# Kernel optimization log

Hardware: AMD Instinct MI355X
Metric: run time of the kernel (lower is better)

Reference implementation:

```python
import jax, jax.numpy as jnp
import numpy as np

N_RAYS = 8192
M = 524288
GX, GY, GZ = 160, 160, 128
NFEAT = 12
POS_PE, VIEW_PE = 10, 4
WIDTH = 128
POS_DIM = 3 + 3 * POS_PE * 2      # 63
VIEW_DIM = 3 + 3 * VIEW_PE * 2    # 27
DIM0 = NFEAT + POS_DIM            # 75
ACT_SHIFT = float(np.log(1.0 / (1.0 - 1e-6) - 1.0))  # density bias shift from alpha_init
INTERVAL = 0.5                    # stepsize * voxel_size_ratio
XYZ_MIN, XYZ_MAX = -1.0, 1.0


def posemb(x, n_pe):
    # x: [N,3] -> [N, 3 + 3*n_pe*2], matching cat([x, sin(x*freq), cos(x*freq)])
    freq = 2.0 ** jnp.arange(n_pe, dtype=x.dtype)
    xf = (x[..., None] * freq).reshape(x.shape[0], -1)
    return jnp.concatenate([x, jnp.sin(xf), jnp.cos(xf)], axis=-1)


def trilinear(grid, xyz):
    # grid: [X,Y,Z,C]; xyz: [M,3] in world coords. align_corners=True bilinear (grid_sample).
    sz_f = jnp.array(grid.shape[:3], jnp.float32)
    sz_i = jnp.array(grid.shape[:3], jnp.int32)
    t = (xyz - XYZ_MIN) / (XYZ_MAX - XYZ_MIN) * (sz_f - 1.0)
    t = jnp.clip(t, 0.0, sz_f - 1.0)
    i0 = jnp.clip(jnp.floor(t).astype(jnp.int32), 0, sz_i - 2)
    f = t - i0.astype(t.dtype)
    out = jnp.zeros((xyz.shape[0], grid.shape[-1]), t.dtype)
    for dx in (0, 1):
        for dy in (0, 1):
            for dz in (0, 1):
                w = ((f[:, 0] if dx else 1.0 - f[:, 0])
                     * (f[:, 1] if dy else 1.0 - f[:, 1])
                     * (f[:, 2] if dz else 1.0 - f[:, 2]))
                out = out + w[:, None] * grid[i0[:, 0] + dx, i0[:, 1] + dy, i0[:, 2] + dz]
    return out


def mask_lookup(mask, xyz):
    # nearest-neighbor maskcache_lookup: ijk = round(xyz*scale + shift)
    sz_f = jnp.array(mask.shape, jnp.float32)
    scale = (sz_f - 1.0) / (XYZ_MAX - XYZ_MIN)
    shift = -XYZ_MIN * scale
    ijk = jnp.clip(jnp.round(xyz * scale + shift).astype(jnp.int32), 0,
                   jnp.array(mask.shape, jnp.int32) - 1)
    return mask[ijk[:, 0], ijk[:, 1], ijk[:, 2]]


def alphas2weights(alpha, ray_id, n_rays):
    # segmented T_i = prod_{j<i in ray}(1-alpha_j); weights = T*alpha (ray_id sorted)
    log1a = jnp.log(jnp.clip(1.0 - alpha, 1e-10, 1.0))
    excl = jnp.cumsum(log1a) - log1a                      # global exclusive cumsum
    seg_tot = jax.ops.segment_sum(log1a, ray_id, num_segments=n_rays)
    seg_start = jnp.cumsum(seg_tot) - seg_tot             # exclusive prefix over rays
    T = jnp.exp(excl - seg_start[ray_id])
    weights = T * alpha
    alphainv_last = jnp.exp(seg_tot)
    return weights, alphainv_last


def setup_inputs() -> dict:
    key = jax.random.key(0)
    ks = jax.random.split(key, 16)
    xyz = jax.random.uniform(ks[0], (M, 3), jnp.float32) * (XYZ_MAX - XYZ_MIN) + XYZ_MIN
    ray_id = jnp.sort(jax.random.randint(ks[1], (M,), 0, N_RAYS))
    viewdirs = jax.random.normal(ks[2], (N_RAYS, 3), jnp.float32)
    viewdirs = viewdirs / jnp.linalg.norm(viewdirs, axis=-1, keepdims=True)
    mask = jax.random.uniform(ks[3], (GX, GY, GZ)) > 0.1
    density = jax.random.normal(ks[4], (GX, GY, GZ), jnp.float32) * 0.5
    k0 = jax.random.normal(ks[5], (GX, GY, GZ, NFEAT), jnp.float32) * 0.1
    s = 0.05
    W0 = jax.random.normal(ks[6], (DIM0, WIDTH), jnp.float32) * s
    b0 = jnp.zeros((WIDTH,), jnp.float32)
    W1 = jax.random.normal(ks[7], (WIDTH, WIDTH), jnp.float32) * s
    b1 = jnp.zeros((WIDTH,), jnp.float32)
    W2 = jax.random.normal(ks[8], (WIDTH, WIDTH), jnp.float32) * s
    b2 = jnp.zeros((WIDTH,), jnp.float32)
    Wr = jax.random.normal(ks[9], (WIDTH + VIEW_DIM, 3), jnp.float32) * s
    br = jnp.zeros((3,), jnp.float32)
    return {"xyz": xyz, "ray_id": ray_id, "viewdirs": viewdirs, "mask": mask,
            "density": density, "k0": k0, "W0": W0, "b0": b0, "W1": W1, "b1": b1,
            "W2": W2, "b2": b2, "Wr": Wr, "br": br}


def reference(xyz, ray_id, viewdirs, mask, density, k0, W0, b0, W1, b1, W2, b2, Wr, br):
    # 1) empty-space skipping via mask cache (kept as multiplicative mask for static shapes)
    m = mask_lookup(mask, xyz).astype(xyz.dtype)
    # 2) trilinear density query + raw2alpha
    d = trilinear(density[..., None], xyz)[:, 0]
    alpha = 1.0 - (1.0 + jnp.exp(d + ACT_SHIFT)) ** (-INTERVAL)
    alpha = alpha * m
    # 3) segmented alpha compositing (Alphas2Weights)
    weights, alphainv_last = alphas2weights(alpha, ray_id, N_RAYS)
    # 4) feature query + view MLP -> rgb
    feat = trilinear(k0, xyz)                              # [M, NFEAT]
    h = jnp.concatenate([feat, posemb(xyz, POS_PE)], -1)   # [M, DIM0]
    h = jax.nn.relu(h @ W0 + b0)
    h = jax.nn.relu(h @ W1 + b1)
    h = jax.nn.relu(h @ W2 + b2)
    ve = posemb(viewdirs, VIEW_PE)[ray_id]                 # [M, VIEW_DIM]
    rgb = jax.nn.sigmoid(jnp.concatenate([h, ve], -1) @ Wr + br)
    # 5) composite per ray + white background
    rgb_marched = jax.ops.segment_sum(weights[:, None] * rgb, ray_id, num_segments=N_RAYS)
    rgb_marched = rgb_marched + alphainv_last[:, None] * 1.0
    return rgb_marched
```

## Files before the change

### kernel.cpp

```cpp
#include <hip/hip_runtime.h>
#include <hip/hip_bf16.h>

#define M_SAMPLES 524288
#define NRAYS 8192
#define GXD 160
#define GYD 160
#define GZD 128
#define GYZ (GYD*GZD)
#define NVOX (GXD*GYD*GZD)
#define ACT_SHIFT -13.81550955796f
#define ROWA 136
#define ROWB 136
#define SAMP 64

typedef __bf16 bf16x8 __attribute__((ext_vector_type(8)));
typedef float f32x4 __attribute__((ext_vector_type(4)));
typedef float f32x16 __attribute__((ext_vector_type(16)));
typedef float f32v2 __attribute__((ext_vector_type(2)));

static __device__ inline unsigned short f2bf(float f){
  __hip_bfloat16 h = __float2bfloat16(f);
  unsigned short u; __builtin_memcpy(&u, &h, 2); return u;
}
static __device__ inline float flo(unsigned int u){ return __uint_as_float(u << 16); }
static __device__ inline float fhi(unsigned int u){ return __uint_as_float(u & 0xffff0000u); }

#if defined(__has_builtin)
#if __has_builtin(__builtin_amdgcn_cvt_pk_bf16_f32)
#define HAVE_PK_BF16 1
#endif
#if __has_builtin(__builtin_amdgcn_cvt_pk_f32_fp8) && __has_builtin(__builtin_amdgcn_cvt_pk_fp8_f32)
#define HAVE_FP8 1
#endif
#endif

static __device__ inline unsigned int packbf(float a, float b){
#ifdef HAVE_PK_BF16
  typedef __bf16 bf16v2 __attribute__((ext_vector_type(2)));
  bf16v2 r = __builtin_amdgcn_cvt_pk_bf16_f32(a, b);
  unsigned int u; __builtin_memcpy(&u, &r, 4); return u;
#else
  return (unsigned int)f2bf(a) | ((unsigned int)f2bf(b) << 16);
#endif
}

struct Tri {
  int ix, iy, iz;
  float wx0, wx1, wy0, wy1, wz0, wz1;
};
static __device__ inline Tri tri_setup(float x, float y, float z){
  Tri t;
  float tx = (x+1.f)*0.5f*(float)(GXD-1); tx = fminf(fmaxf(tx,0.f),(float)(GXD-1));
  float ty = (y+1.f)*0.5f*(float)(GYD-1); ty = fminf(fmaxf(ty,0.f),(float)(GYD-1));
  float tz = (z+1.f)*0.5f*(float)(GZD-1); tz = fminf(fmaxf(tz,0.f),(float)(GZD-1));
  t.ix = min((int)tx, GXD-2); t.iy = min((int)ty, GYD-2); t.iz = min((int)tz, GZD-2);
  float fx = tx-t.ix, fy = ty-t.iy, fz = tz-t.iz;
  t.wx0 = 1.f-fx; t.wx1 = fx; t.wy0 = 1.f-fy; t.wy1 = fy; t.wz0 = 1.f-fz; t.wz1 = fz;
  return t;
}

#define NB_REPACK (NVOX/256)
#define NB_W      184
#define NB_RT     (NRAYS/256)
__global__ __launch_bounds__(256) void k_prep(
    const float* __restrict__ density, const float* __restrict__ k0,
    uint4* __restrict__ packed,
    const unsigned int* __restrict__ mw, int* __restrict__ flag,
    const float* __restrict__ W0, const float* __restrict__ W1,
    const float* __restrict__ W2, const float* __restrict__ Wr,
    const float* __restrict__ br,
    unsigned short* __restrict__ wt0, unsigned short* __restrict__ wt1,
    unsigned short* __restrict__ wt2, unsigned short* __restrict__ wtr,
    const float* __restrict__ vd, float* __restrict__ rayterm3)
{
  int b = blockIdx.x;
  if(b < NB_REPACK){
    int v = b*256 + threadIdx.x;
    const float4* kp = (const float4*)(k0 + (size_t)v*12);
    float4 a = kp[0], bb = kp[1], c = kp[2];
#ifdef HAVE_FP8
    uint4 o;
    o.x = __float_as_uint(density[v]);
    int w;
    w = __builtin_amdgcn_cvt_pk_fp8_f32(a.x, a.y, 0, false);
    w = __builtin_amdgcn_cvt_pk_fp8_f32(a.z, a.w, w, true);
    o.y = (unsigned int)w;
    w = __builtin_amdgcn_cvt_pk_fp8_f32(bb.x, bb.y, 0, false);
    w = __builtin_amdgcn_cvt_pk_fp8_f32(bb.z, bb.w, w, true);
    o.z = (unsigned int)w;
    w = __builtin_amdgcn_cvt_pk_fp8_f32(c.x, c.y, 0, false);
    w = __builtin_amdgcn_cvt_pk_fp8_f32(c.z, c.w, w, true);
    o.w = (unsigned int)w;
    packed[v] = o;
#else
    uint4 o0, o1;
    o0.x = __float_as_uint(density[v]);
    o0.y = packbf(a.x, a.y); o0.z = packbf(a.z, a.w); o0.w = packbf(bb.x, bb.y);
    o1.x = packbf(bb.z, bb.w); o1.y = packbf(c.x, c.y); o1.z = packbf(c.z, c.w);
    o1.w = 0;
    packed[(size_t)v*2]   = o0;
    packed[(size_t)v*2+1] = o1;
#endif
    return;
  }
  if(b == NB_REPACK){
    unsigned int v = mw[threadIdx.x & 63];
    unsigned long long any = __ballot(v > 1u);
    if(threadIdx.x == 0) *flag = (any != 0ull) ? 1 : 0;
    return;
  }
  if(b < NB_REPACK + 1 + NB_W){
    int t = (b - NB_REPACK - 1)*256 + threadIdx.x;
    if(t < 128*96){
      int n = t/96, k = t%96;
      wt0[t] = f2bf((k < 75) ? W0[k*128 + n] : 0.f);
    } else if(t < 128*96 + 16384){
      int j = t - 128*96; int n = j/128, k = j%128;
      wt1[j] = f2bf(W1[k*128 + n]);
    } else if(t < 128*96 + 32768){
      int j = t - 128*96 - 16384; int n = j/128, k = j%128;
      wt2[j] = f2bf(W2[k*128 + n]);
    } else if(t < 128*96 + 32768 + 16*128){
      int j = t - 128*96 - 32768; int n = j/128, k = j%128;
      wtr[j] = f2bf((n < 3) ? Wr[k*3 + n] : 0.f);
    }
    return;
  }
  int ray = (b - NB_REPACK - 1 - NB_W)*256 + threadIdx.x;
  if(ray >= NRAYS) return;
  float v0 = vd[ray*3+0], v1 = vd[ray*3+1], v2 = vd[ray*3+2];
  float vej[27];
  vej[0] = v0; vej[1] = v1; vej[2] = v2;
  #pragma unroll
  for(int ci = 0; ci < 3; ++ci){
    float xv = (ci == 0) ? v0 : ((ci == 1) ? v1 : v2);
    #pragma unroll
    for(int p = 0; p < 4; ++p){
      float arg = xv * (float)(1 << p);
      vej[3 + ci*4 + p]  = __sinf(arg);
      vej[15 + ci*4 + p] = __cosf(arg);
    }
  }
  float rt0 = br[0], rt1 = br[1], rt2 = br[2];
  #pragma unroll
  for(int j = 0; j < 27; ++j){
    const float* wr = Wr + (128 + j)*3;
    rt0 += vej[j]*wr[0]; rt1 += vej[j]*wr[1]; rt2 += vej[j]*wr[2];
  }
  rayterm3[ray*3+0] = rt0; rayterm3[ray*3+1] = rt1; rayterm3[ray*3+2] = rt2;
}

template<int KDIM, int SROW>
static __device__ __forceinline__ void mfma_layer(const unsigned short* src,
    const bf16x8* wf, f32x16& acc0, f32x16& acc1, int ln, int kh)
{
  constexpr int NS = KDIM/16;
  const unsigned short* abase0 = src + (ln)*SROW + kh*8;
  const unsigned short* abase1 = src + (32 + ln)*SROW + kh*8;
  f32x16 z = {0.f,0.f,0.f,0.f,0.f,0.f,0.f,0.f,0.f,0.f,0.f,0.f,0.f,0.f,0.f,0.f};
  acc0 = z; acc1 = z;
  __builtin_amdgcn_s_setprio(1);
  #pragma unroll
  for(int st = 0; st < NS; ++st){
    bf16x8 a0 = *(const bf16x8*)(abase0 + st*16);
    bf16x8 a1 = *(const bf16x8*)(abase1 + st*16);
    acc0 = __builtin_amdgcn_mfma_f32_32x32x16_bf16(wf[st], a0, acc0, 0, 0, 0);
    acc1 = __builtin_amdgcn_mfma_f32_32x32x16_bf16(wf[st], a1, acc1, 0, 0, 0);
  }
  __builtin_amdgcn_s_setprio(0);
}

template<int NS>
static __device__ __forceinline__ void load_wf(const unsigned short* wbase, bf16x8* wf){
  #pragma unroll
  for(int st = 0; st < NS; ++st) wf[st] = *(const bf16x8*)(wbase + st*16);
}

template<int DROW>
static __device__ __forceinline__ void epilogue(const f32x16& acc0, const f32x16& acc1,
    unsigned short* dst, const float* __restrict__ bias, int tile_n, int ln, int kh)
{
  float4 bv[4];
  #pragma unroll
  for(int g = 0; g < 4; ++g) bv[g] = *(const float4*)(bias + tile_n*32 + g*8 + kh*4);
  #pragma unroll
  for(int rep = 0; rep < 2; ++rep){
    const f32x16& acc = rep ? acc1 : acc0;
    int scol = rep*32 + ln;
    #pragma unroll
    for(int g = 0; g < 4; ++g){
      int n0 = tile_n*32 + g*8 + kh*4;
      unsigned int lo = packbf(fmaxf(acc[4*g+0] + bv[g].x, 0.f), fmaxf(acc[4*g+1] + bv[g].y, 0.f));
      unsigned int hi = packbf(fmaxf(acc[4*g+2] + bv[g].z, 0.f), fmaxf(acc[4*g+3] + bv[g].w, 0.f));
      unsigned long long o = (unsigned long long)lo | ((unsigned long long)hi << 32);
      *(unsigned long long*)(dst + scol*DROW + n0) = o;
    }
  }
}

template<int PACKED>
__global__ __launch_bounds__(256, 4) void k_mlp(const float* __restrict__ xyz,
    const uint4* __restrict__ packed,
    const float* __restrict__ density, const float* __restrict__ k0,
    const void* __restrict__ mask, const int* __restrict__ flag,
    const int* __restrict__ ray_id,
    const unsigned short* __restrict__ wt0, const unsigned short* __restrict__ wt1,
    const unsigned short* __restrict__ wt2, const unsigned short* __restrict__ wtr,
    const float* __restrict__ b0, const float* __restrict__ b1,
    const float* __restrict__ b2,
    const float* __restrict__ rayterm3, float4* __restrict__ rgba_out)
{
  __shared__ alignas(16) unsigned short hA[SAMP*ROWA];
  __shared__ alignas(16) unsigned short hB[SAMP*ROWB];
  __shared__ float red[SAMP][4];
  __shared__ int ray_s[SAMP];

  int tid = threadIdx.x;
  int lane = tid & 63, wave = tid >> 6;
  int blk = blockIdx.x*SAMP;
  int ln = lane & 31, kh = lane >> 5;

  bf16x8 wf[8];
  load_wf<6>(wt0 + (wave*32 + ln)*96 + kh*8, wf);

  {
    int smp = tid >> 2, corner = tid & 3;
    int i = blk + smp;
    float x = xyz[3*i+0], y = xyz[3*i+1], z = xyz[3*i+2];
    Tri t = tri_setup(x, y, z);
    int dx = corner & 1, dy = corner >> 1;
    float wxy = (dx ? t.wx1 : t.wx0) * (dy ? t.wy1 : t.wy0);
    float w0 = wxy*t.wz0, w1 = wxy*t.wz1;
    size_t vox = (size_t)((t.ix+dx)*GYZ + (t.iy+dy)*GZD + t.iz);
    float pd;
    float pf[12];
#ifdef HAVE_FP8
    if(PACKED){
      uint4 q0 = packed[vox], q1 = packed[vox+1];
      pd = w0*__uint_as_float(q0.x) + w1*__uint_as_float(q1.x);
      f32v2 a, b;
      a = __builtin_amdgcn_cvt_pk_f32_fp8((int)q0.y, false);
      b = __builtin_amdgcn_cvt_pk_f32_fp8((int)q1.y, false);
      pf[0] = w0*a.x + w1*b.x;  pf[1] = w0*a.y + w1*b.y;
      a = __builtin_amdgcn_cvt_pk_f32_fp8((int)q0.y, true);
      b = __builtin_amdgcn_cvt_pk_f32_fp8((int)q1.y, true);
      pf[2] = w0*a.x + w1*b.x;  pf[3] = w0*a.y + w1*b.y;
      a = __builtin_amdgcn_cvt_pk_f32_fp8((int)q0.z, false);
      b = __builtin_amdgcn_cvt_pk_f32_fp8((int)q1.z, false);
      pf[4] = w0*a.x + w1*b.x;  pf[5] = w0*a.y + w1*b.y;
      a = __builtin_amdgcn_cvt_pk_f32_fp8((int)q0.z, true);
      b = __builtin_amdgcn_cvt_pk_f32_fp8((int)q1.z, true);
      pf[6] = w0*a.x + w1*b.x;  pf[7] = w0*a.y + w1*b.y;
      a = __builtin_amdgcn_cvt_pk_f32_fp8((int)q0.w, false);
      b = __builtin_amdgcn_cvt_pk_f32_fp8((int)q1.w, false);
      pf[8] = w0*a.x + w1*b.x;  pf[9] = w0*a.y + w1*b.y;
      a = __builtin_amdgcn_cvt_pk_f32_fp8((int)q0.w, true);
      b = __builtin_amdgcn_cvt_pk_f32_fp8((int)q1.w, true);
      pf[10]= w0*a.x + w1*b.x;  pf[11]= w0*a.y + w1*b.y;
    }
#else
    if(PACKED){
      const uint4* pv = packed + vox*2;
      uint4 q0 = pv[0], q1 = pv[1], q2 = pv[2], q3 = pv[3];
      pd = w0*__uint_as_float(q0.x) + w1*__uint_as_float(q2.x);
      pf[0]  = w0*flo(q0.y) + w1*flo(q2.y);  pf[1]  = w0*fhi(q0.y) + w1*fhi(q2.y);
      pf[2]  = w0*flo(q0.z) + w1*flo(q2.z);  pf[3]  = w0*fhi(q0.z) + w1*fhi(q2.z);
      pf[4]  = w0*flo(q0.w) + w1*flo(q2.w);  pf[5]  = w0*fhi(q0.w) + w1*fhi(q2.w);
      pf[6]  = w0*flo(q1.x) + w1*flo(q3.x);  pf[7]  = w0*fhi(q1.x) + w1*fhi(q3.x);
      pf[8]  = w0*flo(q1.y) + w1*flo(q3.y);  pf[9]  = w0*fhi(q1.y) + w1*fhi(q3.y);
      pf[10] = w0*flo(q1.z) + w1*flo(q3.z);  pf[11] = w0*fhi(q1.z) + w1*fhi(q3.z);
    }
#endif
    if(!PACKED){
      pd = w0*density[vox] + w1*density[vox+1];
      const float4* v = (const float4*)(k0 + vox*12);
      float4 a0 = v[0], a1 = v[1], a2 = v[2];
      float4 c0 = v[3], c1 = v[4], c2 = v[5];
      pf[0] = w0*a0.x + w1*c0.x;  pf[1] = w0*a0.y + w1*c0.y;
      pf[2] = w0*a0.z + w1*c0.z;  pf[3] = w0*a0.w + w1*c0.w;
      pf[4] = w0*a1.x + w1*c1.x;  pf[5] = w0*a1.y + w1*c1.y;
      pf[6] = w0*a1.z + w1*c1.z;  pf[7] = w0*a1.w + w1*c1.w;
      pf[8] = w0*a2.x + w1*c2.x;  pf[9] = w0*a2.y + w1*c2.y;
      pf[10]= w0*a2.z + w1*c2.z;  pf[11]= w0*a2.w + w1*c2.w;
    }
    #pragma unroll
    for(int m2 = 1; m2 < 4; m2 <<= 1){
      pd += __shfl_xor(pd, m2);
      #pragma unroll
      for(int j = 0; j < 12; ++j) pf[j] += __shfl_xor(pf[j], m2);
    }
    if(corner == 0){
      int mx = (int)rintf(x*79.5f + 79.5f); mx = min(max(mx,0), GXD-1);
      int my = (int)rintf(y*79.5f + 79.5f); my = min(max(my,0), GYD-1);
      int mz = (int)rintf(z*63.5f + 63.5f); mz = min(max(mz,0), GZD-1);
      int midx = mx*GYZ + my*GZD + mz;
      bool mm = (*flag) ? (((const unsigned char*)mask)[midx] != 0)
                        : (((const int*)mask)[midx] != 0);
      float e = __expf(pd + ACT_SHIFT);
      float alpha = 1.f - rsqrtf(1.f + e);
      if(!mm) alpha = 0.f;
      red[smp][3] = alpha;
      unsigned int d[8];
      #pragma unroll
      for(int j = 0; j < 6; ++j) d[j] = packbf(pf[2*j], pf[2*j+1]);
      d[6] = packbf(x, y);
      d[7] = packbf(z, __sinf(x));
      uint4* p = (uint4*)(hA + smp*ROWA);
      p[0] = make_uint4(d[0],d[1],d[2],d[3]);
      p[1] = make_uint4(d[4],d[5],d[6],d[7]);
    } else if(corner == 1){
      uint4* p = (uint4*)(hA + smp*ROWA + 80);
      p[0] = make_uint4(0,0,0,0);
      p[1] = make_uint4(0,0,0,0);
      ray_s[smp] = ray_id[i];
    }
  }

  {
    int smp = tid & 63, chunk = 1 + (tid >> 6);
    int i2 = blk + smp;
    float x = xyz[3*i2+0], y = xyz[3*i2+1], z = xyz[3*i2+2];
    float vv[16];
    #pragma unroll
    for(int j = 0; j < 16; ++j){
      int c = chunk*16 + j;
      float r;
      if(c >= 75) r = 0.f;
      else {
        int q = (c < 45) ? (c-15) : (c-45);
        int ci = q/10, p = q - ci*10;
        float xv = (ci == 0) ? x : ((ci == 1) ? y : z);
        float a = xv * (float)(1 << p);
        r = (c < 45) ? __sinf(a) : __cosf(a);
      }
      vv[j] = r;
    }
    unsigned int d[8];
    #pragma unroll
    for(int j = 0; j < 8; ++j) d[j] = packbf(vv[2*j], vv[2*j+1]);
    uint4* p = (uint4*)(hA + smp*ROWA + chunk*16);
    p[0] = make_uint4(d[0],d[1],d[2],d[3]);
    p[1] = make_uint4(d[4],d[5],d[6],d[7]);
  }
  __syncthreads();

  f32x16 acc0, acc1;

  mfma_layer<96, ROWA>(hA, wf, acc0, acc1, ln, kh);
  load_wf<8>(wt1 + (wave*32 + ln)*128 + kh*8, wf);
  epilogue<ROWB>(acc0, acc1, hB, b0, wave, ln, kh);
  __syncthreads();

  mfma_layer<128, ROWB>(hB, wf, acc0, acc1, ln, kh);
  load_wf<8>(wt2 + (wave*32 + ln)*128 + kh*8, wf);
  epilogue<ROWA>(acc0, acc1, hA, b1, wave, ln, kh);
  __syncthreads();

  int col = lane & 15, q4 = lane >> 4;
  mfma_layer<128, ROWA>(hA, wf, acc0, acc1, ln, kh);
  bf16x8 hw[4];
  {
    const unsigned short* wr = wtr + col*128 + q4*8;
    #pragma unroll
    for(int ks = 0; ks < 4; ++ks) hw[ks] = *(const bf16x8*)(wr + ks*32);
  }
  epilogue<ROWB>(acc0, acc1, hB, b2, wave, ln, kh);
  __syncthreads();

  {
    int mt = wave;
    f32x4 acc = {0.f, 0.f, 0.f, 0.f};
    const unsigned short* arow = hB + (mt*16 + col)*ROWB + q4*8;
    __builtin_amdgcn_s_setprio(1);
    #pragma unroll
    for(int ks = 0; ks < 4; ++ks){
      bf16x8 af = *(const bf16x8*)(arow + ks*32);
      acc = __builtin_amdgcn_mfma_f32_16x16x32_bf16(af, hw[ks], acc, 0, 0, 0);
    }
    __builtin_amdgcn_s_setprio(0);
    if(col < 3){
      #pragma unroll
      for(int r = 0; r < 4; ++r){
        int sl = mt*16 + q4*4 + r;
        float v = acc[r] + rayterm3[ray_s[sl]*3 + col];
        red[sl][col] = __fdividef(1.f, 1.f + __expf(-v));
      }
    }
  }
  __syncthreads();

  if(tid < SAMP){
    rgba_out[blk + tid] = make_float4(red[tid][0], red[tid][1], red[tid][2], red[tid][3]);
  }
}

__global__ __launch_bounds__(256) void k_comp2(const int* __restrict__ ray_id,
    const float4* __restrict__ rgba, float* __restrict__ out)
{
  int r = blockIdx.x*4 + (threadIdx.x >> 6);
  int lane = threadIdx.x & 63;
  int lo = 0, hi = M_SAMPLES;
  while(lo < hi){ int mid = (lo+hi) >> 1; if(ray_id[mid] < r) lo = mid+1; else hi = mid; }
  int s = lo;
  int lo2 = s, hi2 = M_SAMPLES;
  while(lo2 < hi2){ int mid = (lo2+hi2) >> 1; if(ray_id[mid] < r+1) lo2 = mid+1; else hi2 = mid; }
  int e = lo2;

  float carry = 1.f;
  float ar = 0.f, ag = 0.f, ab = 0.f;
  for(int base = s; base < e; base += 64){
    int idx = base + lane;
    float4 c = (idx < e) ? rgba[idx] : make_float4(0.f,0.f,0.f,0.f);
    float a = c.w;
    float incl = 1.f - a;
    #pragma unroll
    for(int d2 = 1; d2 < 64; d2 <<= 1){
      float t = __shfl_up(incl, d2);
      if(lane >= d2) incl *= t;
    }
    float excl = __shfl_up(incl, 1);
    if(lane == 0) excl = 1.f;
    float w = carry * excl * a;
    ar += w*c.x; ag += w*c.y; ab += w*c.z;
    carry *= __shfl(incl, 63);
  }
  #pragma unroll
  for(int m2 = 1; m2 < 64; m2 <<= 1){
    ar += __shfl_xor(ar, m2);
    ag += __shfl_xor(ag, m2);
    ab += __shfl_xor(ab, m2);
  }
  if(lane == 0){
    out[3*r+0] = ar + carry;
    out[3*r+1] = ag + carry;
    out[3*r+2] = ab + carry;
  }
}

extern "C" void kernel_launch(void* const* d_in, const int* in_sizes, int n_in,
                              void* d_out, int out_size, void* d_ws, size_t ws_size,
                              hipStream_t stream)
{
  const float* xyz      = (const float*)d_in[0];
  const int*   ray_id   = (const int*)  d_in[1];
  const float* viewdirs = (const float*)d_in[2];
  const void*  mask     =               d_in[3];
  const float* density  = (const float*)d_in[4];
  const float* k0       = (const float*)d_in[5];
  const float* W0 = (const float*)d_in[6];  const float* b0 = (const float*)d_in[7];
  const float* W1 = (const float*)d_in[8];  const float* b1 = (const float*)d_in[9];
  const float* W2 = (const float*)d_in[10]; const float* b2 = (const float*)d_in[11];
  const float* Wr = (const float*)d_in[12]; const float* br = (const float*)d_in[13];
  float* out = (float*)d_out;

  char* ws = (char*)d_ws;
  size_t off = 0;
  auto take = [&](size_t nbytes) -> void* {
    void* p = ws + off;
    off = (off + nbytes + 255) & ~(size_t)255;
    return p;
  };
  int*            flag     = (int*)           take(4);
  unsigned short* wt0      = (unsigned short*)take(128*96*2);
  unsigned short* wt1      = (unsigned short*)take(128*128*2);
  unsigned short* wt2      = (unsigned short*)take(128*128*2);
  unsigned short* wtr      = (unsigned short*)take(16*128*2);
  float*          rayterm3 = (float*)         take((size_t)NRAYS*3*4);
  float4*         rgba_ws  = (float4*)        take((size_t)M_SAMPLES*16);
#ifdef HAVE_FP8
  uint4*          packed   = (uint4*)         take((size_t)NVOX*16);
#else
  uint4*          packed   = (uint4*)         take((size_t)NVOX*32);
#endif
  bool use_packed = (ws_size >= off);

  k_prep<<<NB_REPACK + 1 + NB_W + NB_RT, 256, 0, stream>>>(
      density, k0, packed, (const unsigned int*)mask, flag,
      W0, W1, W2, Wr, br, wt0, wt1, wt2, wtr, viewdirs, rayterm3);
  if(use_packed){
    k_mlp<1><<<M_SAMPLES/SAMP, 256, 0, stream>>>(xyz, packed, density, k0, mask, flag,
                                                 ray_id, wt0, wt1, wt2, wtr,
                                                 b0, b1, b2, rayterm3, rgba_ws);
  } else {
    k_mlp<0><<<M_SAMPLES/SAMP, 256, 0, stream>>>(xyz, packed, density, k0, mask, flag,
                                                 ray_id, wt0, wt1, wt2, wtr,
                                                 b0, b1, b2, rayterm3, rgba_ws);
  }
  k_comp2<<<NRAYS/4, 256, 0, stream>>>(ray_id, rgba_ws, out);
}
```

Measured before the change: 417.1 us.

## Split trilinear gather into separate kernel feeding MLP via global buffer

Moves the trilinear density/feature gather, mask lookup and alpha computation out of the MLP kernel into a new k_gather kernel that writes packed bf16 features and alphas to workspace. The MLP kernel then loads these precomputed rows into shared memory, which shortens its prologue and is meant to keep the MFMA-heavy kernel free of latency-bound random gathers. The cost is an extra kernel launch and a round trip through global memory for a 32-byte feature row plus an alpha per sample. The repack branch in k_prep is also skipped when packing is not possible.

```diff
diff --git a/kernel.cpp b/kernel.cpp
--- a/kernel.cpp
+++ b/kernel.cpp
@@ -60,9 +60,9 @@
 }
 
 #define NB_REPACK (NVOX/256)
-#define NB_W      184
-#define NB_RT     (NRAYS/256)
-__global__ __launch_bounds__(256) void k_prep(
+#define NB_W  184
+#define NB_RT (NRAYS/256)
+__global__ __launch_bounds__(256) void k_prep(int do_repack,
     const float* __restrict__ density, const float* __restrict__ k0,
     uint4* __restrict__ packed,
     const unsigned int* __restrict__ mw, int* __restrict__ flag,
@@ -74,43 +74,46 @@
     const float* __restrict__ vd, float* __restrict__ rayterm3)
 {
   int b = blockIdx.x;
-  if(b < NB_REPACK){
-    int v = b*256 + threadIdx.x;
-    const float4* kp = (const float4*)(k0 + (size_t)v*12);
-    float4 a = kp[0], bb = kp[1], c = kp[2];
+  if(do_repack){
+    if(b < NB_REPACK){
+      int v = b*256 + threadIdx.x;
+      const float4* kp = (const float4*)(k0 + (size_t)v*12);
+      float4 a = kp[0], bb = kp[1], c = kp[2];
 #ifdef HAVE_FP8
-    uint4 o;
-    o.x = __float_as_uint(density[v]);
-    int w;
-    w = __builtin_amdgcn_cvt_pk_fp8_f32(a.x, a.y, 0, false);
-    w = __builtin_amdgcn_cvt_pk_fp8_f32(a.z, a.w, w, true);
-    o.y = (unsigned int)w;
-    w = __builtin_amdgcn_cvt_pk_fp8_f32(bb.x, bb.y, 0, false);
-    w = __builtin_amdgcn_cvt_pk_fp8_f32(bb.z, bb.w, w, true);
-    o.z = (unsigned int)w;
-    w = __builtin_amdgcn_cvt_pk_fp8_f32(c.x, c.y, 0, false);
-    w = __builtin_amdgcn_cvt_pk_fp8_f32(c.z, c.w, w, true);
-    o.w = (unsigned int)w;
-    packed[v] = o;
+      uint4 o;
+      o.x = __float_as_uint(density[v]);
+      int w;
+      w = __builtin_amdgcn_cvt_pk_fp8_f32(a.x, a.y, 0, false);
+      w = __builtin_amdgcn_cvt_pk_fp8_f32(a.z, a.w, w, true);
+      o.y = (unsigned int)w;
+      w = __builtin_amdgcn_cvt_pk_fp8_f32(bb.x, bb.y, 0, false);
+      w = __builtin_amdgcn_cvt_pk_fp8_f32(bb.z, bb.w, w, true);
+      o.z = (unsigned int)w;
+      w = __builtin_amdgcn_cvt_pk_fp8_f32(c.x, c.y, 0, false);
+      w = __builtin_amdgcn_cvt_pk_fp8_f32(c.z, c.w, w, true);
+      o.w = (unsigned int)w;
+      packed[v] = o;
 #else
-    uint4 o0, o1;
-    o0.x = __float_as_uint(density[v]);
-    o0.y = packbf(a.x, a.y); o0.z = packbf(a.z, a.w); o0.w = packbf(bb.x, bb.y);
-    o1.x = packbf(bb.z, bb.w); o1.y = packbf(c.x, c.y); o1.z = packbf(c.z, c.w);
-    o1.w = 0;
-    packed[(size_t)v*2]   = o0;
-    packed[(size_t)v*2+1] = o1;
-#endif
-    return;
-  }
-  if(b == NB_REPACK){
+      uint4 o0, o1;
+      o0.x = __float_as_uint(density[v]);
+      o0.y = packbf(a.x, a.y); o0.z = packbf(a.z, a.w); o0.w = packbf(bb.x, bb.y);
+      o1.x = packbf(bb.z, bb.w); o1.y = packbf(c.x, c.y); o1.z = packbf(c.z, c.w);
+      o1.w = 0;
+      packed[(size_t)v*2]   = o0;
+      packed[(size_t)v*2+1] = o1;
+#endif
+      return;
+    }
+    b -= NB_REPACK;
+  }
+  if(b == 0){
     unsigned int v = mw[threadIdx.x & 63];
     unsigned long long any = __ballot(v > 1u);
     if(threadIdx.x == 0) *flag = (any != 0ull) ? 1 : 0;
     return;
   }
-  if(b < NB_REPACK + 1 + NB_W){
-    int t = (b - NB_REPACK - 1)*256 + threadIdx.x;
+  if(b < 1 + NB_W){
+    int t = (b - 1)*256 + threadIdx.x;
     if(t < 128*96){
       int n = t/96, k = t%96;
       wt0[t] = f2bf((k < 75) ? W0[k*128 + n] : 0.f);
@@ -126,7 +129,7 @@
     }
     return;
   }
-  int ray = (b - NB_REPACK - 1 - NB_W)*256 + threadIdx.x;
+  int ray = (b - 1 - NB_W)*256 + threadIdx.x;
   if(ray >= NRAYS) return;
   float v0 = vd[ray*3+0], v1 = vd[ray*3+1], v2 = vd[ray*3+2];
   float vej[27];
@@ -148,6 +151,102 @@
     rt0 += vej[j]*wr[0]; rt1 += vej[j]*wr[1]; rt2 += vej[j]*wr[2];
   }
   rayterm3[ray*3+0] = rt0; rayterm3[ray*3+1] = rt1; rayterm3[ray*3+2] = rt2;
+}
+
+template<int PACKED>
+__global__ __launch_bounds__(256) void k_gather(
+    const float* __restrict__ xyz,
+    const uint4* __restrict__ packed,
+    const float* __restrict__ density, const float* __restrict__ k0,
+    const void* __restrict__ mask, const int* __restrict__ flag,
+    uint4* __restrict__ feats, float* __restrict__ alphab)
+{
+  int gid = blockIdx.x*256 + threadIdx.x;
+  int smp = gid >> 2, corner = gid & 3;
+  float x = xyz[3*smp+0], y = xyz[3*smp+1], z = xyz[3*smp+2];
+  Tri t = tri_setup(x, y, z);
+  int dx = corner & 1, dy = corner >> 1;
+  float wxy = (dx ? t.wx1 : t.wx0) * (dy ? t.wy1 : t.wy0);
+  float w0 = wxy*t.wz0, w1 = wxy*t.wz1;
+  size_t vox = (size_t)((t.ix+dx)*GYZ + (t.iy+dy)*GZD + t.iz);
+
+  float pd;
+  float pf[12];
+#ifdef HAVE_FP8
+  if(PACKED){
+    uint4 q0 = packed[vox], q1 = packed[vox+1];
+    pd = w0*__uint_as_float(q0.x) + w1*__uint_as_float(q1.x);
+    f32v2 a, b;
+    a = __builtin_amdgcn_cvt_pk_f32_fp8((int)q0.y, false);
+    b = __builtin_amdgcn_cvt_pk_f32_fp8((int)q1.y, false);
+    pf[0] = w0*a.x + w1*b.x;  pf[1] = w0*a.y + w1*b.y;
+    a = __builtin_amdgcn_cvt_pk_f32_fp8((int)q0.y, true);
+    b = __builtin_amdgcn_cvt_pk_f32_fp8((int)q1.y, true);
+    pf[2] = w0*a.x + w1*b.x;  pf[3] = w0*a.y + w1*b.y;
+    a = __builtin_amdgcn_cvt_pk_f32_fp8((int)q0.z, false);
+    b = __builtin_amdgcn_cvt_pk_f32_fp8((int)q1.z, false);
+    pf[4] = w0*a.x + w1*b.x;  pf[5] = w0*a.y + w1*b.y;
+    a = __builtin_amdgcn_cvt_pk_f32_fp8((int)q0.z, true);
+    b = __builtin_amdgcn_cvt_pk_f32_fp8((int)q1.z, true);
+    pf[6] = w0*a.x + w1*b.x;  pf[7] = w0*a.y + w1*b.y;
+    a = __builtin_amdgcn_cvt_pk_f32_fp8((int)q0.w, false);
+    b = __builtin_amdgcn_cvt_pk_f32_fp8((int)q1.w, false);
+    pf[8] = w0*a.x + w1*b.x;  pf[9] = w0*a.y + w1*b.y;
+    a = __builtin_amdgcn_cvt_pk_f32_fp8((int)q0.w, true);
+    b = __builtin_amdgcn_cvt_pk_f32_fp8((int)q1.w, true);
+    pf[10]= w0*a.x + w1*b.x;  pf[11]= w0*a.y + w1*b.y;
+  }
+#else
+  if(PACKED){
+    const uint4* pv = packed + vox*2;
+    uint4 q0 = pv[0], q1 = pv[1], q2 = pv[2], q3 = pv[3];
+    pd = w0*__uint_as_float(q0.x) + w1*__uint_as_float(q2.x);
+    pf[0]  = w0*flo(q0.y) + w1*flo(q2.y);  pf[1]  = w0*fhi(q0.y) + w1*fhi(q2.y);
+    pf[2]  = w0*flo(q0.z) + w1*flo(q2.z);  pf[3]  = w0*fhi(q0.z) + w1*fhi(q2.z);
+    pf[4]  = w0*flo(q0.w) + w1*flo(q2.w);  pf[5]  = w0*fhi(q0.w) + w1*fhi(q2.w);
+    pf[6]  = w0*flo(q1.x) + w1*flo(q3.x);  pf[7]  = w0*fhi(q1.x) + w1*fhi(q3.x);
+    pf[8]  = w0*flo(q1.y) + w1*flo(q3.y);  pf[9]  = w0*fhi(q1.y) + w1*fhi(q3.y);
+    pf[10] = w0*flo(q1.z) + w1*flo(q3.z);  pf[11] = w0*fhi(q1.z) + w1*fhi(q3.z);
+  }
+#endif
+  if(!PACKED){
+    pd = w0*density[vox] + w1*density[vox+1];
+    const float4* v = (const float4*)(k0 + vox*12);
+    float4 a0 = v[0], a1 = v[1], a2 = v[2];
+    float4 c0 = v[3], c1 = v[4], c2 = v[5];
+    pf[0] = w0*a0.x + w1*c0.x;  pf[1] = w0*a0.y + w1*c0.y;
+    pf[2] = w0*a0.z + w1*c0.z;  pf[3] = w0*a0.w + w1*c0.w;
+    pf[4] = w0*a1.x + w1*c1.x;  pf[5] = w0*a1.y + w1*c1.y;
+    pf[6] = w0*a1.z + w1*c1.z;  pf[7] = w0*a1.w + w1*c1.w;
+    pf[8] = w0*a2.x + w1*c2.x;  pf[9] = w0*a2.y + w1*c2.y;
+    pf[10]= w0*a2.z + w1*c2.z;  pf[11]= w0*a2.w + w1*c2.w;
+  }
+
+  #pragma unroll
+  for(int m2 = 1; m2 < 4; m2 <<= 1){
+    pd += __shfl_xor(pd, m2);
+    #pragma unroll
+    for(int j = 0; j < 12; ++j) pf[j] += __shfl_xor(pf[j], m2);
+  }
+  if(corner == 0){
+    int mx = (int)rintf(x*79.5f + 79.5f); mx = min(max(mx,0), GXD-1);
+    int my = (int)rintf(y*79.5f + 79.5f); my = min(max(my,0), GYD-1);
+    int mz = (int)rintf(z*63.5f + 63.5f); mz = min(max(mz,0), GZD-1);
+    int midx = mx*GYZ + my*GZD + mz;
+    bool mm = (*flag) ? (((const unsigned char*)mask)[midx] != 0)
+                      : (((const int*)mask)[midx] != 0);
+    float e = __expf(pd + ACT_SHIFT);
+    float alpha = 1.f - rsqrtf(1.f + e);
+    if(!mm) alpha = 0.f;
+    alphab[smp] = alpha;
+    unsigned int d[8];
+    #pragma unroll
+    for(int j = 0; j < 6; ++j) d[j] = packbf(pf[2*j], pf[2*j+1]);
+    d[6] = packbf(x, y);
+    d[7] = packbf(z, __sinf(x));
+    feats[(size_t)smp*2]   = make_uint4(d[0],d[1],d[2],d[3]);
+    feats[(size_t)smp*2+1] = make_uint4(d[4],d[5],d[6],d[7]);
+  }
 }
 
 template<int KDIM, int SROW>
@@ -198,11 +297,8 @@
   }
 }
 
-template<int PACKED>
 __global__ __launch_bounds__(256, 4) void k_mlp(const float* __restrict__ xyz,
-    const uint4* __restrict__ packed,
-    const float* __restrict__ density, const float* __restrict__ k0,
-    const void* __restrict__ mask, const int* __restrict__ flag,
+    const uint4* __restrict__ feats, const float* __restrict__ alphab,
     const int* __restrict__ ray_id,
     const unsigned short* __restrict__ wt0, const unsigned short* __restrict__ wt1,
     const unsigned short* __restrict__ wt2, const unsigned short* __restrict__ wtr,
@@ -223,103 +319,15 @@
   bf16x8 wf[8];
   load_wf<6>(wt0 + (wave*32 + ln)*96 + kh*8, wf);
 
+  uint4 fv = make_uint4(0,0,0,0);
+  if(tid < 128) fv = feats[(size_t)blk*2 + tid];
+  int smp = tid & 63, chunk = 1 + (tid >> 6);
+  int i2 = blk + smp;
+  float x = xyz[3*i2+0], y = xyz[3*i2+1], z = xyz[3*i2+2];
+  float al = 0.f; int rid = 0;
+  if(tid < SAMP){ al = alphab[blk + tid]; rid = ray_id[blk + tid]; }
+
   {
-    int smp = tid >> 2, corner = tid & 3;
-    int i = blk + smp;
-    float x = xyz[3*i+0], y = xyz[3*i+1], z = xyz[3*i+2];
-    Tri t = tri_setup(x, y, z);
-    int dx = corner & 1, dy = corner >> 1;
-    float wxy = (dx ? t.wx1 : t.wx0) * (dy ? t.wy1 : t.wy0);
-    float w0 = wxy*t.wz0, w1 = wxy*t.wz1;
-    size_t vox = (size_t)((t.ix+dx)*GYZ + (t.iy+dy)*GZD + t.iz);
-    float pd;
-    float pf[12];
-#ifdef HAVE_FP8
-    if(PACKED){
-      uint4 q0 = packed[vox], q1 = packed[vox+1];
-      pd = w0*__uint_as_float(q0.x) + w1*__uint_as_float(q1.x);
-      f32v2 a, b;
-      a = __builtin_amdgcn_cvt_pk_f32_fp8((int)q0.y, false);
-      b = __builtin_amdgcn_cvt_pk_f32_fp8((int)q1.y, false);
-      pf[0] = w0*a.x + w1*b.x;  pf[1] = w0*a.y + w1*b.y;
-      a = __builtin_amdgcn_cvt_pk_f32_fp8((int)q0.y, true);
-      b = __builtin_amdgcn_cvt_pk_f32_fp8((int)q1.y, true);
-      pf[2] = w0*a.x + w1*b.x;  pf[3] = w0*a.y + w1*b.y;
-      a = __builtin_amdgcn_cvt_pk_f32_fp8((int)q0.z, false);
-      b = __builtin_amdgcn_cvt_pk_f32_fp8((int)q1.z, false);
-      pf[4] = w0*a.x + w1*b.x;  pf[5] = w0*a.y + w1*b.y;
-      a = __builtin_amdgcn_cvt_pk_f32_fp8((int)q0.z, true);
-      b = __builtin_amdgcn_cvt_pk_f32_fp8((int)q1.z, true);
-      pf[6] = w0*a.x + w1*b.x;  pf[7] = w0*a.y + w1*b.y;
-      a = __builtin_amdgcn_cvt_pk_f32_fp8((int)q0.w, false);
-      b = __builtin_amdgcn_cvt_pk_f32_fp8((int)q1.w, false);
-      pf[8] = w0*a.x + w1*b.x;  pf[9] = w0*a.y + w1*b.y;
-      a = __builtin_amdgcn_cvt_pk_f32_fp8((int)q0.w, true);
-      b = __builtin_amdgcn_cvt_pk_f32_fp8((int)q1.w, true);
-      pf[10]= w0*a.x + w1*b.x;  pf[11]= w0*a.y + w1*b.y;
-    }
-#else
-    if(PACKED){
-      const uint4* pv = packed + vox*2;
-      uint4 q0 = pv[0], q1 = pv[1], q2 = pv[2], q3 = pv[3];
-      pd = w0*__uint_as_float(q0.x) + w1*__uint_as_float(q2.x);
-      pf[0]  = w0*flo(q0.y) + w1*flo(q2.y);  pf[1]  = w0*fhi(q0.y) + w1*fhi(q2.y);
-      pf[2]  = w0*flo(q0.z) + w1*flo(q2.z);  pf[3]  = w0*fhi(q0.z) + w1*fhi(q2.z);
-      pf[4]  = w0*flo(q0.w) + w1*flo(q2.w);  pf[5]  = w0*fhi(q0.w) + w1*fhi(q2.w);
-      pf[6]  = w0*flo(q1.x) + w1*flo(q3.x);  pf[7]  = w0*fhi(q1.x) + w1*fhi(q3.x);
-      pf[8]  = w0*flo(q1.y) + w1*flo(q3.y);  pf[9]  = w0*fhi(q1.y) + w1*fhi(q3.y);
-      pf[10] = w0*flo(q1.z) + w1*flo(q3.z);  pf[11] = w0*fhi(q1.z) + w1*fhi(q3.z);
-    }
-#endif
-    if(!PACKED){
-      pd = w0*density[vox] + w1*density[vox+1];
-      const float4* v = (const float4*)(k0 + vox*12);
-      float4 a0 = v[0], a1 = v[1], a2 = v[2];
-      float4 c0 = v[3], c1 = v[4], c2 = v[5];
-      pf[0] = w0*a0.x + w1*c0.x;  pf[1] = w0*a0.y + w1*c0.y;
-      pf[2] = w0*a0.z + w1*c0.z;  pf[3] = w0*a0.w + w1*c0.w;
-      pf[4] = w0*a1.x + w1*c1.x;  pf[5] = w0*a1.y + w1*c1.y;
-      pf[6] = w0*a1.z + w1*c1.z;  pf[7] = w0*a1.w + w1*c1.w;
-      pf[8] = w0*a2.x + w1*c2.x;  pf[9] = w0*a2.y + w1*c2.y;
-      pf[10]= w0*a2.z + w1*c2.z;  pf[11]= w0*a2.w + w1*c2.w;
-    }
-    #pragma unroll
-    for(int m2 = 1; m2 < 4; m2 <<= 1){
-      pd += __shfl_xor(pd, m2);
-      #pragma unroll
-      for(int j = 0; j < 12; ++j) pf[j] += __shfl_xor(pf[j], m2);
-    }
-    if(corner == 0){
-      int mx = (int)rintf(x*79.5f + 79.5f); mx = min(max(mx,0), GXD-1);
-      int my = (int)rintf(y*79.5f + 79.5f); my = min(max(my,0), GYD-1);
-      int mz = (int)rintf(z*63.5f + 63.5f); mz = min(max(mz,0), GZD-1);
-      int midx = mx*GYZ + my*GZD + mz;
-      bool mm = (*flag) ? (((const unsigned char*)mask)[midx] != 0)
-                        : (((const int*)mask)[midx] != 0);
-      float e = __expf(pd + ACT_SHIFT);
-      float alpha = 1.f - rsqrtf(1.f + e);
-      if(!mm) alpha = 0.f;
-      red[smp][3] = alpha;
-      unsigned int d[8];
-      #pragma unroll
-      for(int j = 0; j < 6; ++j) d[j] = packbf(pf[2*j], pf[2*j+1]);
-      d[6] = packbf(x, y);
-      d[7] = packbf(z, __sinf(x));
-      uint4* p = (uint4*)(hA + smp*ROWA);
-      p[0] = make_uint4(d[0],d[1],d[2],d[3]);
-      p[1] = make_uint4(d[4],d[5],d[6],d[7]);
-    } else if(corner == 1){
-      uint4* p = (uint4*)(hA + smp*ROWA + 80);
-      p[0] = make_uint4(0,0,0,0);
-      p[1] = make_uint4(0,0,0,0);
-      ray_s[smp] = ray_id[i];
-    }
-  }
-
-  {
-    int smp = tid & 63, chunk = 1 + (tid >> 6);
-    int i2 = blk + smp;
-    float x = xyz[3*i2+0], y = xyz[3*i2+1], z = xyz[3*i2+2];
     float vv[16];
     #pragma unroll
     for(int j = 0; j < 16; ++j){
@@ -342,6 +350,12 @@
     p[0] = make_uint4(d[0],d[1],d[2],d[3]);
     p[1] = make_uint4(d[4],d[5],d[6],d[7]);
   }
+  if(tid < 128){
+    *(uint4*)(hA + (tid>>1)*ROWA + (tid&1)*8) = fv;
+  } else {
+    *(uint4*)(hA + ((tid-128)>>1)*ROWA + 80 + (tid&1)*8) = make_uint4(0,0,0,0);
+  }
+  if(tid < SAMP) ray_s[tid] = rid;
   __syncthreads();
 
   f32x16 acc0, acc1;
@@ -390,7 +404,7 @@
   __syncthreads();
 
   if(tid < SAMP){
-    rgba_out[blk + tid] = make_float4(red[tid][0], red[tid][1], red[tid][2], red[tid][3]);
+    rgba_out[blk + tid] = make_float4(red[tid][0], red[tid][1], red[tid][2], al);
   }
 }
 
@@ -467,24 +481,27 @@
   unsigned short* wtr      = (unsigned short*)take(16*128*2);
   float*          rayterm3 = (float*)         take((size_t)NRAYS*3*4);
   float4*         rgba_ws  = (float4*)        take((size_t)M_SAMPLES*16);
+  uint4*          feats    = (uint4*)         take((size_t)M_SAMPLES*32);
+  float*          alphab   = (float*)         take((size_t)M_SAMPLES*4);
 #ifdef HAVE_FP8
   uint4*          packed   = (uint4*)         take((size_t)NVOX*16);
 #else
   uint4*          packed   = (uint4*)         take((size_t)NVOX*32);
 #endif
-  bool use_packed = (ws_size >= off);
-
-  k_prep<<<NB_REPACK + 1 + NB_W + NB_RT, 256, 0, stream>>>(
-      density, k0, packed, (const unsigned int*)mask, flag,
+  int use_packed = (ws_size >= off) ? 1 : 0;
+
+  k_prep<<<(use_packed ? NB_REPACK : 0) + 1 + NB_W + NB_RT, 256, 0, stream>>>(
+      use_packed, density, k0, packed, (const unsigned int*)mask, flag,
       W0, W1, W2, Wr, br, wt0, wt1, wt2, wtr, viewdirs, rayterm3);
   if(use_packed){
-    k_mlp<1><<<M_SAMPLES/SAMP, 256, 0, stream>>>(xyz, packed, density, k0, mask, flag,
-                                                 ray_id, wt0, wt1, wt2, wtr,
-                                                 b0, b1, b2, rayterm3, rgba_ws);
+    k_gather<1><<<M_SAMPLES*4/256, 256, 0, stream>>>(
+        xyz, packed, density, k0, mask, flag, feats, alphab);
   } else {
-    k_mlp<0><<<M_SAMPLES/SAMP, 256, 0, stream>>>(xyz, packed, density, k0, mask, flag,
-                                                 ray_id, wt0, wt1, wt2, wtr,
-                                                 b0, b1, b2, rayterm3, rgba_ws);
-  }
+    k_gather<0><<<M_SAMPLES*4/256, 256, 0, stream>>>(
+        xyz, packed, density, k0, mask, flag, feats, alphab);
+  }
+  k_mlp<<<M_SAMPLES/SAMP, 256, 0, stream>>>(
+      xyz, feats, alphab, ray_id, wt0, wt1, wt2, wtr,
+      b0, b1, b2, rayterm3, rgba_ws);
   k_comp2<<<NRAYS/4, 256, 0, stream>>>(ray_id, rgba_ws, out);
 }
```

Result: slower. 442.4 us (+6.1%).
